# Kernel tuning notes

Measured on AMD Instinct MI355X. Metric: run time of the kernel, lower is better.

The kernel has to match this reference:

```python
import jax, jax.numpy as jnp
import numpy as np

EMBED_DIM = 512
NUM_HEADS = 8
WINDOW = 5
OVERLAP = 1
STRIDE = WINDOW - OVERLAP  # 4


def setup_inputs() -> dict:
    key = jax.random.key(0)
    ks = jax.random.split(key, 5)
    B, S, D = 8, 4096, EMBED_DIM
    s = 1.0 / np.sqrt(D).astype(np.float32)
    return {
        "x": jax.random.normal(ks[0], (B, S, D), jnp.float32),
        "Wq": jax.random.normal(ks[1], (D, D), jnp.float32) * s,
        "bq": jnp.zeros((D,), jnp.float32),
        "Wk": jax.random.normal(ks[2], (D, D), jnp.float32) * s,
        "bk": jnp.zeros((D,), jnp.float32),
        "Wv": jax.random.normal(ks[3], (D, D), jnp.float32) * s,
        "bv": jnp.zeros((D,), jnp.float32),
        "Wo": jax.random.normal(ks[4], (D, D), jnp.float32) * s,
        "bo": jnp.zeros((D,), jnp.float32),
    }


def reference(x, Wq, bq, Wk, bk, Wv, bv, Wo, bo):
    B, S, D = x.shape
    H = NUM_HEADS
    hd = D // H
    pad = (WINDOW - S % WINDOW) % WINDOW
    xp = jnp.pad(x, ((0, 0), (0, pad), (0, 0)))
    P = S + pad
    nw = (P - WINDOW) // STRIDE + 1

    # gather all sliding windows at once: [B, nw, W, D]
    idx = (jnp.arange(nw) * STRIDE)[:, None] + jnp.arange(WINDOW)  # [nw, W]
    win = xp[:, idx]

    def proj(t, W, b):
        return (t @ W + b).reshape(B, nw, WINDOW, H, hd)

    q = proj(win, Wq, bq)
    k = proj(win, Wk, bk)
    v = proj(win, Wv, bv)

    scale = jnp.float32(1.0 / np.sqrt(hd))
    scores = jnp.einsum('bnqhd,bnkhd->bnhqk', q, k) * scale  # [B,nw,H,W,W]
    attn = jax.nn.softmax(scores, axis=-1)
    o = jnp.einsum('bnhqk,bnkhd->bnqhd', attn, v).reshape(B, nw, WINDOW, D)
    o = o @ Wo + bo  # window outputs [B,nw,W,D]

    # overlap-add + count-average (exactly as the torch loop does)
    flat_idx = idx.reshape(-1)
    out = jnp.zeros((B, P, D), jnp.float32).at[:, flat_idx].add(
        o.reshape(B, nw * WINDOW, D))
    counts = jnp.zeros((P,), jnp.float32).at[flat_idx].add(1.0)
    out = out / (counts[None, :, None] + 1e-6)
    out = out[:, :S]

    # torch: sum(all_weights) / num_windows  -> mean over window axis
    attn_weights = attn.mean(axis=1)  # [B, H, W, W]
    return out, attn_weights
```

## Files before the change

kernel.cpp:

```cpp
#include <hip/hip_runtime.h>
#include <hip/hip_bf16.h>


#define SEQ   4096
#define NB    8
#define DIM   512
#define NWIN  1024
#define MTOT  (NB*SEQ)

typedef __bf16 bf16x8 __attribute__((ext_vector_type(8)));
typedef float  f32x4  __attribute__((ext_vector_type(4)));

__device__ __forceinline__ float b2f(unsigned short u) {
  union { unsigned int i; float f; } z; z.i = ((unsigned int)u) << 16; return z.f;
}
__device__ __forceinline__ unsigned short f2b(float f) {
  __bf16 h = (__bf16)f; return __builtin_bit_cast(unsigned short, h);
}
__device__ __forceinline__ void gload_lds16(const void* g, void* l) {
  __builtin_amdgcn_global_load_lds(
      (__attribute__((address_space(1))) void*)g,
      (__attribute__((address_space(3))) void*)l, 16, 0, 0);
}

#define FENCE() asm volatile("" ::: "memory")
#define BAR()   __builtin_amdgcn_s_barrier()
#define LGK0()  asm volatile("s_waitcnt lgkmcnt(0)" ::: "memory")
#define VMW4()  asm volatile("s_waitcnt vmcnt(4)" ::: "memory")
#define VMW0()  asm volatile("s_waitcnt vmcnt(0)" ::: "memory")

__global__ __launch_bounds__(256) void cvt_x(const float* __restrict__ x,
                                             unsigned short* __restrict__ o, int n8) {
  int stride = gridDim.x * blockDim.x;
  for (int i = blockIdx.x * blockDim.x + threadIdx.x; i < n8; i += stride) {
    const float4 a = *(const float4*)(x + (size_t)i * 8);
    const float4 c = *(const float4*)(x + (size_t)i * 8 + 4);
    unsigned short u[8] = {f2b(a.x), f2b(a.y), f2b(a.z), f2b(a.w),
                           f2b(c.x), f2b(c.y), f2b(c.z), f2b(c.w)};
    *(int4*)(o + (size_t)i * 8) = *(const int4*)u;
  }
}

__global__ __launch_bounds__(256) void cvt_w(const float* __restrict__ W0, const float* __restrict__ W1,
                                             const float* __restrict__ W2, const float* __restrict__ W3,
                                             unsigned short* __restrict__ Wt) {
  int i = blockIdx.x * 256 + threadIdx.x;
  int w = i >> 18;
  int r = i & 262143;
  int nn = r >> 9, kk = r & 511;
  const float* W = (w == 0) ? W0 : (w == 1) ? W1 : (w == 2) ? W2 : W3;
  Wt[i] = f2b(W[kk * 512 + nn]);
}

__device__ __forceinline__ void stage_part(int h, const unsigned short* pa, const unsigned short* pb,
    int r0s, int c0s, int r1s, int c1s, char* ldsb, int wid) {
  int kt = h >> 2, slot = (h + 2) & 3;
  int buf = kt & 1, ab = slot >> 1, half = slot & 1;
  const unsigned short* src = ab ? pb : pa;
  int rb = half << 7;
  int kc = kt << 6;
  char* d = ldsb + buf * 65536 + ab * 32768 + half * 16384 + wid * 1024;
  gload_lds16(src + (size_t)(rb + r0s) * 512 + kc + c0s, d);
  gload_lds16(src + (size_t)(rb + r1s) * 512 + kc + c1s, d + 8192);
}

#define LDSB(off) (*(const bf16x8*)(ldsb + (off)))

#define RA4(BUF, HALF) { \
  _Pragma("unroll") for (int mf2 = 0; mf2 < 4; ++mf2) { \
    _Pragma("unroll") for (int ks = 0; ks < 2; ++ks) \
      a[mf2][ks] = LDSB(aS[BUF][ks] + (HALF) * 8192 + mf2 * 2048); } }

#define RB2(BUF, QN) { \
  _Pragma("unroll") for (int nf2 = 0; nf2 < 2; ++nf2) { \
    _Pragma("unroll") for (int ks = 0; ks < 2; ++ks) \
      b[(QN)*2+nf2][ks] = LDSB(bS[BUF][ks] + (QN) * 4096 + nf2 * 2048); } }

#define MMQ(QM, QN) { \
  _Pragma("unroll") for (int ks = 0; ks < 2; ++ks) \
  _Pragma("unroll") for (int mf2 = 0; mf2 < 4; ++mf2) \
  _Pragma("unroll") for (int nf2 = 0; nf2 < 2; ++nf2) \
    acc[(QM)*4+mf2][(QN)*2+nf2] = __builtin_amdgcn_mfma_f32_16x16x32_bf16( \
      a[mf2][ks], b[(QN)*2+nf2][ks], acc[(QM)*4+mf2][(QN)*2+nf2], 0, 0, 0); }

template<int MODE>
__global__ __launch_bounds__(512, 2) void gemm8(
    const unsigned short* __restrict__ A, const unsigned short* __restrict__ Bw,
    const float* __restrict__ b0, const float* __restrict__ b1, const float* __restrict__ b2,
    unsigned short* __restrict__ o0, unsigned short* __restrict__ o1, unsigned short* __restrict__ o2,
    float* __restrict__ fout) {
  __shared__ unsigned short lds_[65536];
  char* ldsb = (char*)lds_;

  const int nwg = gridDim.x;
  const int cpx = nwg >> 3;
  const int g = blockIdx.x;
  const int sw = (g & 7) * cpx + (g >> 3);
  constexpr int NTN = (MODE == 0) ? 6 : 2;
  const int ntile = sw % NTN, mtile = sw / NTN;
  const int m0 = mtile * 256, n0g = ntile * 256;

  const int tid = threadIdx.x;
  const int lane = tid & 63;
  const int wid = tid >> 6;
  const int wr = wid >> 2, wc = wid & 3;
  const int cl16 = lane & 15, hi = lane >> 4;
  const int hi16 = hi * 16;
  const int sxor = (cl16 & 14) << 3;

  int o0_ = tid * 16;
  int o1_ = 8192 + tid * 16;
  int l0 = o0_ ^ (((o0_ >> 8) & 7) << 4);
  int l1 = o1_ ^ (((o1_ >> 8) & 7) << 4);
  const int r0s = l0 >> 7, c0s = (l0 & 127) >> 1;
  const int r1s = l1 >> 7, c1s = (l1 & 127) >> 1;

  const unsigned short* pa = A + (size_t)m0 * 512;
  const unsigned short* pb = Bw + (size_t)n0g * 512;

  int aS[2][2], bS[2][2];
#pragma unroll
  for (int bu = 0; bu < 2; ++bu)
#pragma unroll
    for (int ks = 0; ks < 2; ++ks) {
      aS[bu][ks] = bu * 65536 + ((wr * 16384 + cl16 * 128 + ks * 64 + hi16) ^ sxor);
      bS[bu][ks] = bu * 65536 + 32768 + (((wc >> 1) * 16384 + (wc & 1) * 8192 + cl16 * 128 + ks * 64 + hi16) ^ sxor);
    }

  f32x4 acc[8][4] = {};
  bf16x8 a[4][2], b[4][2];

#define STG(H) stage_part((H), pa, pb, r0s, c0s, r1s, c1s, ldsb, wid)

  STG(0); STG(1); STG(2); STG(3); STG(4); STG(5);
  VMW4();
  FENCE(); BAR();

#pragma unroll
  for (int it = 0; it < 4; ++it) {
    const int hb = 8 * it;
    RA4(0, 0); RB2(0, 0);
    STG(hb + 6);
    FENCE(); BAR();
    __builtin_amdgcn_s_setprio(1); MMQ(0, 0); __builtin_amdgcn_s_setprio(0);
    FENCE(); BAR();
    RB2(0, 1);
    if (hb + 7 < 32) STG(hb + 7);
    FENCE(); BAR();
    __builtin_amdgcn_s_setprio(1); MMQ(0, 1); __builtin_amdgcn_s_setprio(0);
    FENCE(); BAR();
    RA4(0, 1);
    if (it < 3) STG(hb + 8);
    FENCE(); BAR();
    __builtin_amdgcn_s_setprio(1); MMQ(1, 1); __builtin_amdgcn_s_setprio(0);
    FENCE(); BAR();
    if (it < 3) STG(hb + 9);
    FENCE(); BAR();
    __builtin_amdgcn_s_setprio(1); MMQ(1, 0); __builtin_amdgcn_s_setprio(0);
    if (it < 3) { VMW4(); } else { VMW0(); }
    FENCE(); BAR();
    RA4(1, 0); RB2(1, 0);
    if (it < 3) STG(hb + 10);
    FENCE(); BAR();
    __builtin_amdgcn_s_setprio(1); MMQ(0, 0); __builtin_amdgcn_s_setprio(0);
    FENCE(); BAR();
    RB2(1, 1);
    if (it < 3) STG(hb + 11);
    FENCE(); BAR();
    __builtin_amdgcn_s_setprio(1); MMQ(0, 1); __builtin_amdgcn_s_setprio(0);
    FENCE(); BAR();
    RA4(1, 1);
    if (it < 3) STG(hb + 12);
    FENCE(); BAR();
    __builtin_amdgcn_s_setprio(1); MMQ(1, 1); __builtin_amdgcn_s_setprio(0);
    FENCE(); BAR();
    if (it < 3) STG(hb + 13);
    FENCE(); BAR();
    __builtin_amdgcn_s_setprio(1); MMQ(1, 0); __builtin_amdgcn_s_setprio(0);
    if (it < 3) { VMW4(); }
    FENCE(); BAR();
  }

  if constexpr (MODE == 0) {
    const int sel = n0g >> 9;
    const float* bias = (sel == 0) ? b0 : (sel == 1) ? b1 : b2;
    unsigned short* C = (sel == 0) ? o0 : (sel == 1) ? o1 : o2;
    const int lcb = (n0g & 511) + wc * 64;
    unsigned short* wlds = lds_ + wid * 8192;
#pragma unroll
    for (int mf = 0; mf < 8; ++mf)
#pragma unroll
      for (int nf = 0; nf < 4; ++nf) {
        float bv_ = bias[lcb + nf * 16 + cl16];
#pragma unroll
        for (int r = 0; r < 4; ++r) {
          int w = (mf * 16 + hi * 4 + r) * 64 + nf * 16 + cl16;
          wlds[w ^ (((w >> 7) & 7) << 3)] = f2b(acc[mf][nf][r] + bv_);
        }
      }
    LGK0();
#pragma unroll
    for (int itr = 0; itr < 16; ++itr) {
      int f = itr * 512 + lane * 8;
      int row = f >> 6, col = f & 63;
      int4 v = *(const int4*)&wlds[f ^ (((f >> 7) & 7) << 3)];
      *(int4*)(C + (size_t)(m0 + wr * 128 + row) * 512 + lcb + col) = v;
    }
  } else {
#pragma unroll
    for (int nf = 0; nf < 4; ++nf) {
      int ncol = n0g + wc * 64 + nf * 16 + cl16;
      float bv_ = b0[ncol];
#pragma unroll
      for (int mf = 0; mf < 8; ++mf) {
        int rbase = m0 + wr * 128 + mf * 16 + hi * 4;
#pragma unroll
        for (int r = 0; r < 4; ++r) {
          int row = rbase + r;
          int s = row & (SEQ - 1);
          float cnt = ((s & 3) == 0 && s > 0) ? 2.0f : 1.0f;
          fout[(size_t)row * 512 + ncol] = (acc[mf][nf][r] + cnt * bv_) / (cnt + 1e-6f);
        }
      }
    }
  }
}

__global__ __launch_bounds__(256) void attn_win(
    const unsigned short* __restrict__ Qb, const unsigned short* __restrict__ Kb,
    const unsigned short* __restrict__ Vb,
    const float* __restrict__ bq, const float* __restrict__ bk, const float* __restrict__ bv,
    unsigned short* __restrict__ yb, unsigned short* __restrict__ yext,
    float* __restrict__ abuf) {
  const int gw = blockIdx.x * 4 + (threadIdx.x >> 6);
  const int b = gw >> 10, n = gw & (NWIN - 1);
  const int lane = threadIdx.x & 63;
  const int h = lane >> 3, e = lane & 7;
  const int dbase = h * 64 + e * 8;

  float kf[5][8], vf[5][8];
#pragma unroll
  for (int j = 0; j < 5; ++j) {
    int p = 4 * n + j;
    if (p < SEQ) {
      int4 kv = *(const int4*)(Kb + ((size_t)b * SEQ + p) * DIM + dbase);
      int4 vv = *(const int4*)(Vb + ((size_t)b * SEQ + p) * DIM + dbase);
      const unsigned short* kp = (const unsigned short*)&kv;
      const unsigned short* vp = (const unsigned short*)&vv;
#pragma unroll
      for (int d = 0; d < 8; ++d) { kf[j][d] = b2f(kp[d]); vf[j][d] = b2f(vp[d]); }
    } else {
#pragma unroll
      for (int d = 0; d < 8; ++d) { kf[j][d] = bk[dbase + d]; vf[j][d] = bv[dbase + d]; }
    }
  }
  float pm[5][5];
#pragma unroll
  for (int i = 0; i < 5; ++i) {
    int p = 4 * n + i;
    float qf[8];
    if (p < SEQ) {
      int4 qv = *(const int4*)(Qb + ((size_t)b * SEQ + p) * DIM + dbase);
      const unsigned short* qp = (const unsigned short*)&qv;
#pragma unroll
      for (int d = 0; d < 8; ++d) qf[d] = b2f(qp[d]);
    } else {
#pragma unroll
      for (int d = 0; d < 8; ++d) qf[d] = bq[dbase + d];
    }
    float sr[5];
#pragma unroll
    for (int j = 0; j < 5; ++j) {
      float t = 0.f;
#pragma unroll
      for (int d = 0; d < 8; ++d) t += qf[d] * kf[j][d];
      t += __shfl_xor(t, 1);
      t += __shfl_xor(t, 2);
      t += __shfl_xor(t, 4);
      sr[j] = t * 0.125f;
    }
    float mx = sr[0];
#pragma unroll
    for (int j = 1; j < 5; ++j) mx = fmaxf(mx, sr[j]);
    float ex[5], sum = 0.f;
#pragma unroll
    for (int j = 0; j < 5; ++j) { ex[j] = expf(sr[j] - mx); sum += ex[j]; }
    float inv = 1.0f / sum;
#pragma unroll
    for (int j = 0; j < 5; ++j) pm[i][j] = ex[j] * inv;
    float o[8];
#pragma unroll
    for (int d = 0; d < 8; ++d) o[d] = 0.f;
#pragma unroll
    for (int j = 0; j < 5; ++j)
#pragma unroll
      for (int d = 0; d < 8; ++d) o[d] += pm[i][j] * vf[j][d];
    unsigned short u[8];
#pragma unroll
    for (int d = 0; d < 8; ++d) u[d] = f2b(o[d]);
    if (i < 4) {
      *(int4*)(yb + ((size_t)b * SEQ + p) * DIM + dbase) = *(const int4*)u;
    } else {
      *(int4*)(yext + ((size_t)b * NWIN + n) * DIM + dbase) = *(const int4*)u;
    }
  }
  float* ap = abuf + ((size_t)(b * NWIN + n) * 8 + h) * 25;
  if (e == 0) {
#pragma unroll
    for (int i2 = 0; i2 < 5; ++i2)
#pragma unroll
      for (int j2 = 0; j2 < 5; ++j2) ap[i2 * 5 + j2] = pm[i2][j2];
  }
}

__global__ __launch_bounds__(256) void merge_y(unsigned short* __restrict__ y,
                                               const unsigned short* __restrict__ ye) {
  int idx = blockIdx.x * 256 + threadIdx.x;
  if (idx >= 8 * 1023 * 64) return;
  int d8 = idx & 63;
  int t = idx >> 6;
  int n = t % 1023 + 1;
  int b = t / 1023;
  size_t yo = ((size_t)b * SEQ + 4 * (size_t)n) * DIM + d8 * 8;
  size_t eo = ((size_t)b * NWIN + (n - 1)) * DIM + d8 * 8;
  int4 av = *(const int4*)(y + yo);
  int4 cv = *(const int4*)(ye + eo);
  const unsigned short* ap = (const unsigned short*)&av;
  const unsigned short* cp = (const unsigned short*)&cv;
  unsigned short u[8];
#pragma unroll
  for (int j = 0; j < 8; ++j) u[j] = f2b(b2f(ap[j]) + b2f(cp[j]));
  *(int4*)(y + yo) = *(const int4*)u;
}

__global__ __launch_bounds__(256) void attn_reduce(const float* __restrict__ abuf,
                                                   float* __restrict__ out) {
  __shared__ float sm[256][25];
  int bh = blockIdx.x;
  int b = bh >> 3, h = bh & 7;
  int t = threadIdx.x;
  float loc[25];
#pragma unroll
  for (int j = 0; j < 25; ++j) loc[j] = 0.f;
  for (int n = t; n < NWIN; n += 256) {
    const float* p = abuf + ((size_t)(b * NWIN + n) * 8 + h) * 25;
#pragma unroll
    for (int j = 0; j < 25; ++j) loc[j] += p[j];
  }
#pragma unroll
  for (int j = 0; j < 25; ++j) sm[t][j] = loc[j];
  __syncthreads();
  for (int off = 128; off > 0; off >>= 1) {
    if (t < off)
#pragma unroll
      for (int j = 0; j < 25; ++j) sm[t][j] += sm[t + off][j];
    __syncthreads();
  }
  if (t < 25) out[bh * 25 + t] = sm[0][t] * (1.0f / 1024.0f);
}

extern "C" void kernel_launch(void* const* d_in, const int* in_sizes, int n_in,
                              void* d_out, int out_size, void* d_ws, size_t ws_size,
                              hipStream_t stream) {
  const float* x  = (const float*)d_in[0];
  const float* Wq = (const float*)d_in[1];
  const float* bq = (const float*)d_in[2];
  const float* Wk = (const float*)d_in[3];
  const float* bk = (const float*)d_in[4];
  const float* Wv = (const float*)d_in[5];
  const float* bv = (const float*)d_in[6];
  const float* Wo = (const float*)d_in[7];
  const float* bo = (const float*)d_in[8];
  float* out = (float*)d_out;

  char* ws = (char*)d_ws;
  unsigned short* xb   = (unsigned short*)(ws);
  unsigned short* yb   = xb;
  unsigned short* Qb   = (unsigned short*)(ws + 33554432);
  unsigned short* Kb   = (unsigned short*)(ws + 67108864);
  unsigned short* Vb   = (unsigned short*)(ws + 100663296);
  unsigned short* yext = (unsigned short*)(ws + 134217728);
  float*          abuf = (float*)(ws + 142606336);
  unsigned short* Wt   = (unsigned short*)(ws + 149159936);
  (void)ws_size; (void)in_sizes; (void)n_in; (void)out_size;

  cvt_x<<<2048, 256, 0, stream>>>(x, xb, MTOT * DIM / 8);
  cvt_w<<<4096, 256, 0, stream>>>(Wq, Wk, Wv, Wo, Wt);
  gemm8<0><<<768, 512, 0, stream>>>(xb, Wt, bq, bk, bv, Qb, Kb, Vb, nullptr);
  attn_win<<<2048, 256, 0, stream>>>(Qb, Kb, Vb, bq, bk, bv, yb, yext, abuf);
  merge_y<<<2046, 256, 0, stream>>>(yb, yext);
  gemm8<1><<<256, 512, 0, stream>>>(yb, Wt + 3 * (DIM * DIM), bo, nullptr, nullptr,
                                    nullptr, nullptr, nullptr, out);
  attn_reduce<<<64, 256, 0, stream>>>(abuf, out + (size_t)MTOT * DIM);
}
```

Before: 160.5 us.

## Fuse conversion kernels and fold window overlap merge into attention kernel

Merges the x and weight bf16 conversion kernels into one launch, and rewrites the weight transpose through an LDS tile so that global reads and writes are coalesced. The attention kernel now recomputes the previous window's last query row itself and adds it into row 4n. This removes the yext buffer and the separate merge_y kernel, at the cost of redundant K/V loads and score computation per window. It also switches to __expf and remaps blocks so that blocks in the same group of 8 come from different batches.

```diff
diff --git a/kernel.cpp b/kernel.cpp
--- a/kernel.cpp
+++ b/kernel.cpp
@@ -29,27 +29,42 @@
 #define VMW4()  asm volatile("s_waitcnt vmcnt(4)" ::: "memory")
 #define VMW0()  asm volatile("s_waitcnt vmcnt(0)" ::: "memory")
 
-__global__ __launch_bounds__(256) void cvt_x(const float* __restrict__ x,
-                                             unsigned short* __restrict__ o, int n8) {
-  int stride = gridDim.x * blockDim.x;
-  for (int i = blockIdx.x * blockDim.x + threadIdx.x; i < n8; i += stride) {
-    const float4 a = *(const float4*)(x + (size_t)i * 8);
-    const float4 c = *(const float4*)(x + (size_t)i * 8 + 4);
-    unsigned short u[8] = {f2b(a.x), f2b(a.y), f2b(a.z), f2b(a.w),
-                           f2b(c.x), f2b(c.y), f2b(c.z), f2b(c.w)};
-    *(int4*)(o + (size_t)i * 8) = *(const int4*)u;
-  }
-}
-
-__global__ __launch_bounds__(256) void cvt_w(const float* __restrict__ W0, const float* __restrict__ W1,
-                                             const float* __restrict__ W2, const float* __restrict__ W3,
-                                             unsigned short* __restrict__ Wt) {
-  int i = blockIdx.x * 256 + threadIdx.x;
-  int w = i >> 18;
-  int r = i & 262143;
-  int nn = r >> 9, kk = r & 511;
-  const float* W = (w == 0) ? W0 : (w == 1) ? W1 : (w == 2) ? W2 : W3;
-  Wt[i] = f2b(W[kk * 512 + nn]);
+__global__ __launch_bounds__(256) void cvt_fused(
+    const float* __restrict__ x, const float* __restrict__ W0,
+    const float* __restrict__ W1, const float* __restrict__ W2,
+    const float* __restrict__ W3,
+    unsigned short* __restrict__ xb, unsigned short* __restrict__ Wt) {
+  if (blockIdx.x < 2048) {
+    const int n8 = MTOT * DIM / 8;
+    const int stride = 2048 * 256;
+    for (int i = blockIdx.x * 256 + threadIdx.x; i < n8; i += stride) {
+      const float4 a = *(const float4*)(x + (size_t)i * 8);
+      const float4 c = *(const float4*)(x + (size_t)i * 8 + 4);
+      unsigned short u[8] = {f2b(a.x), f2b(a.y), f2b(a.z), f2b(a.w),
+                             f2b(c.x), f2b(c.y), f2b(c.z), f2b(c.w)};
+      *(int4*)(xb + (size_t)i * 8) = *(const int4*)u;
+    }
+  } else {
+    __shared__ float tile[64][65];
+    const int bb = blockIdx.x - 2048;
+    const int w = bb >> 6;
+    const int tr = (bb & 63) >> 3, tc = bb & 7;
+    const float* W = (w == 0) ? W0 : (w == 1) ? W1 : (w == 2) ? W2 : W3;
+    const int c = threadIdx.x & 63, r4 = threadIdx.x >> 6;
+#pragma unroll
+    for (int i = 0; i < 16; ++i) {
+      int r = r4 + i * 4;
+      tile[r][c] = W[(size_t)(tr * 64 + r) * 512 + tc * 64 + c];
+    }
+    __syncthreads();
+    const int kk = threadIdx.x & 63, n4 = threadIdx.x >> 6;
+#pragma unroll
+    for (int i = 0; i < 16; ++i) {
+      int nn = n4 + i * 4;
+      Wt[((size_t)w << 18) + (size_t)(tc * 64 + nn) * 512 + tr * 64 + kk] =
+          f2b(tile[kk][nn]);
+    }
+  }
 }
 
 __device__ __forceinline__ void stage_part(int h, const unsigned short* pa, const unsigned short* pb,
@@ -230,21 +245,66 @@
     const unsigned short* __restrict__ Qb, const unsigned short* __restrict__ Kb,
     const unsigned short* __restrict__ Vb,
     const float* __restrict__ bq, const float* __restrict__ bk, const float* __restrict__ bv,
-    unsigned short* __restrict__ yb, unsigned short* __restrict__ yext,
-    float* __restrict__ abuf) {
-  const int gw = blockIdx.x * 4 + (threadIdx.x >> 6);
+    unsigned short* __restrict__ yb, float* __restrict__ abuf) {
+  const int g = blockIdx.x;
+  const int swg = (g & 7) * 256 + (g >> 3);
+  const int gw = swg * 4 + (threadIdx.x >> 6);
   const int b = gw >> 10, n = gw & (NWIN - 1);
   const int lane = threadIdx.x & 63;
   const int h = lane >> 3, e = lane & 7;
   const int dbase = h * 64 + e * 8;
+  const size_t rowbase = (size_t)b * SEQ;
+
+  float o4[8];
+#pragma unroll
+  for (int d = 0; d < 8; ++d) o4[d] = 0.f;
+  if (n > 0) {
+    float q0[8];
+    {
+      int4 qv = *(const int4*)(Qb + (rowbase + 4 * n) * DIM + dbase);
+      const unsigned short* qp = (const unsigned short*)&qv;
+#pragma unroll
+      for (int d = 0; d < 8; ++d) q0[d] = b2f(qp[d]);
+    }
+    float sc[5];
+#pragma unroll
+    for (int j = 0; j < 5; ++j) {
+      int p = 4 * n - 4 + j;
+      int4 kv = *(const int4*)(Kb + (rowbase + p) * DIM + dbase);
+      const unsigned short* kp = (const unsigned short*)&kv;
+      float t = 0.f;
+#pragma unroll
+      for (int d = 0; d < 8; ++d) t += q0[d] * b2f(kp[d]);
+      t += __shfl_xor(t, 1);
+      t += __shfl_xor(t, 2);
+      t += __shfl_xor(t, 4);
+      sc[j] = t * 0.125f;
+    }
+    float mx = sc[0];
+#pragma unroll
+    for (int j = 1; j < 5; ++j) mx = fmaxf(mx, sc[j]);
+    float ex[5], sum = 0.f;
+#pragma unroll
+    for (int j = 0; j < 5; ++j) { ex[j] = __expf(sc[j] - mx); sum += ex[j]; }
+    float inv = 1.0f / sum;
+#pragma unroll
+    for (int j = 0; j < 5; ++j) {
+      int p = 4 * n - 4 + j;
+      int4 vv = *(const int4*)(Vb + (rowbase + p) * DIM + dbase);
+      const unsigned short* vp = (const unsigned short*)&vv;
+      float wj = ex[j] * inv;
+#pragma unroll
+      for (int d = 0; d < 8; ++d) o4[d] += wj * b2f(vp[d]);
+    }
+  }
 
   float kf[5][8], vf[5][8];
 #pragma unroll
   for (int j = 0; j < 5; ++j) {
     int p = 4 * n + j;
     if (p < SEQ) {
-      int4 kv = *(const int4*)(Kb + ((size_t)b * SEQ + p) * DIM + dbase);
-      int4 vv = *(const int4*)(Vb + ((size_t)b * SEQ + p) * DIM + dbase);
+      int4 kv = *(const int4*)(Kb + (rowbase + p) * DIM + dbase);
+      int4 vv = *(const int4*)(Vb + (rowbase + p) * DIM + dbase);
       const unsigned short* kp = (const unsigned short*)&kv;
       const unsigned short* vp = (const unsigned short*)&vv;
 #pragma unroll
@@ -260,7 +320,7 @@
     int p = 4 * n + i;
     float qf[8];
     if (p < SEQ) {
-      int4 qv = *(const int4*)(Qb + ((size_t)b * SEQ + p) * DIM + dbase);
+      int4 qv = *(const int4*)(Qb + (rowbase + p) * DIM + dbase);
       const unsigned short* qp = (const unsigned short*)&qv;
 #pragma unroll
       for (int d = 0; d < 8; ++d) qf[d] = b2f(qp[d]);
@@ -284,24 +344,22 @@
     for (int j = 1; j < 5; ++j) mx = fmaxf(mx, sr[j]);
     float ex[5], sum = 0.f;
 #pragma unroll
-    for (int j = 0; j < 5; ++j) { ex[j] = expf(sr[j] - mx); sum += ex[j]; }
+    for (int j = 0; j < 5; ++j) { ex[j] = __expf(sr[j] - mx); sum += ex[j]; }
     float inv = 1.0f / sum;
 #pragma unroll
     for (int j = 0; j < 5; ++j) pm[i][j] = ex[j] * inv;
-    float o[8];
-#pragma unroll
-    for (int d = 0; d < 8; ++d) o[d] = 0.f;
-#pragma unroll
-    for (int j = 0; j < 5; ++j)
-#pragma unroll
-      for (int d = 0; d < 8; ++d) o[d] += pm[i][j] * vf[j][d];
-    unsigned short u[8];
-#pragma unroll
-    for (int d = 0; d < 8; ++d) u[d] = f2b(o[d]);
     if (i < 4) {
-      *(int4*)(yb + ((size_t)b * SEQ + p) * DIM + dbase) = *(const int4*)u;
-    } else {
-      *(int4*)(yext + ((size_t)b * NWIN + n) * DIM + dbase) = *(const int4*)u;
+      float o[8];
+#pragma unroll
+      for (int d = 0; d < 8; ++d) o[d] = (i == 0) ? o4[d] : 0.f;
+#pragma unroll
+      for (int j = 0; j < 5; ++j)
+#pragma unroll
+        for (int d = 0; d < 8; ++d) o[d] += pm[i][j] * vf[j][d];
+      unsigned short u[8];
+#pragma unroll
+      for (int d = 0; d < 8; ++d) u[d] = f2b(o[d]);
+      *(int4*)(yb + (rowbase + p) * DIM + dbase) = *(const int4*)u;
     }
   }
   float* ap = abuf + ((size_t)(b * NWIN + n) * 8 + h) * 25;
@@ -311,26 +369,6 @@
 #pragma unroll
       for (int j2 = 0; j2 < 5; ++j2) ap[i2 * 5 + j2] = pm[i2][j2];
   }
-}
-
-__global__ __launch_bounds__(256) void merge_y(unsigned short* __restrict__ y,
-                                               const unsigned short* __restrict__ ye) {
-  int idx = blockIdx.x * 256 + threadIdx.x;
-  if (idx >= 8 * 1023 * 64) return;
-  int d8 = idx & 63;
-  int t = idx >> 6;
-  int n = t % 1023 + 1;
-  int b = t / 1023;
-  size_t yo = ((size_t)b * SEQ + 4 * (size_t)n) * DIM + d8 * 8;
-  size_t eo = ((size_t)b * NWIN + (n - 1)) * DIM + d8 * 8;
-  int4 av = *(const int4*)(y + yo);
-  int4 cv = *(const int4*)(ye + eo);
-  const unsigned short* ap = (const unsigned short*)&av;
-  const unsigned short* cp = (const unsigned short*)&cv;
-  unsigned short u[8];
-#pragma unroll
-  for (int j = 0; j < 8; ++j) u[j] = f2b(b2f(ap[j]) + b2f(cp[j]));
-  *(int4*)(y + yo) = *(const int4*)u;
 }
 
 __global__ __launch_bounds__(256) void attn_reduce(const float* __restrict__ abuf,
@@ -379,16 +417,13 @@
   unsigned short* Qb   = (unsigned short*)(ws + 33554432);
   unsigned short* Kb   = (unsigned short*)(ws + 67108864);
   unsigned short* Vb   = (unsigned short*)(ws + 100663296);
-  unsigned short* yext = (unsigned short*)(ws + 134217728);
   float*          abuf = (float*)(ws + 142606336);
   unsigned short* Wt   = (unsigned short*)(ws + 149159936);
   (void)ws_size; (void)in_sizes; (void)n_in; (void)out_size;
 
-  cvt_x<<<2048, 256, 0, stream>>>(x, xb, MTOT * DIM / 8);
-  cvt_w<<<4096, 256, 0, stream>>>(Wq, Wk, Wv, Wo, Wt);
+  cvt_fused<<<2304, 256, 0, stream>>>(x, Wq, Wk, Wv, Wo, xb, Wt);
   gemm8<0><<<768, 512, 0, stream>>>(xb, Wt, bq, bk, bv, Qb, Kb, Vb, nullptr);
-  attn_win<<<2048, 256, 0, stream>>>(Qb, Kb, Vb, bq, bk, bv, yb, yext, abuf);
-  merge_y<<<2046, 256, 0, stream>>>(yb, yext);
+  attn_win<<<2048, 256, 0, stream>>>(Qb, Kb, Vb, bq, bk, bv, yb, abuf);
   gemm8<1><<<256, 512, 0, stream>>>(yb, Wt + 3 * (DIM * DIM), bo, nullptr, nullptr,
                                     nullptr, nullptr, nullptr, out);
   attn_reduce<<<64, 256, 0, stream>>>(abuf, out + (size_t)MTOT * DIM);
```

Result: faster. 148.3 us (-7.6%).
